# Kernel tuning notes

Hardware: AMD Instinct MI355X
Metric: run time of the kernel (lower is better)

The kernel has to match this reference:

```python
import jax, jax.numpy as jnp
import numpy as np

B, M, P, L, L_EVAL = 16, 32, 16, 1024, 2048


def setup_inputs() -> dict:
    key = jax.random.key(0)
    ks = jax.random.split(key, 6)
    # sorted event times per (B, P) path via cumsum of positive steps
    steps = jax.random.uniform(ks[0], (B, P, L), minval=0.01, maxval=0.1)
    event_times = jnp.cumsum(steps, axis=-1)  # [B, P, L], strictly increasing
    norm_constants = jax.random.uniform(ks[1], (B,), minval=0.5, maxval=1.5)
    # queries on the ORIGINAL (unnormalised) time axis, spanning the event range
    t_max = event_times[..., -1]  # [B, P]
    q_norm = jax.random.uniform(ks[2], (B, P, L_EVAL)) * (1.05 * t_max)[..., None]
    query_times = q_norm * norm_constants[:, None, None]
    mu = jax.random.uniform(ks[3], (B, M, P, L), minval=0.05, maxval=1.0)
    alpha = jax.random.uniform(ks[4], (B, M, P, L), minval=0.05, maxval=2.0)
    beta = jax.random.uniform(ks[5], (B, M, P, L), minval=0.1, maxval=3.0)
    return {
        "query_times": query_times,
        "event_times": event_times,
        "mu": mu,
        "alpha": alpha,
        "beta": beta,
        "norm_constants": norm_constants,
    }


def _batched_searchsorted(a, v):
    # a: [B, P, L] sorted along last dim, v: [B, P, Q] -> int32 [B, P, Q]
    f = lambda av, vv: jnp.searchsorted(av, vv, side="left")
    return jax.vmap(jax.vmap(f))(a, v)


def reference(query_times, event_times, mu, alpha, beta, norm_constants):
    Bq, Pq, Le = query_times.shape
    Mm = mu.shape[1]
    # normalized_times=False path: map queries onto the normalised axis
    q_norm = query_times / norm_constants[:, None, None]  # [B, P, Le]
    # index of the latest event strictly before each query time
    last_idx = _batched_searchsorted(event_times, q_norm) - 1  # [B, P, Le]
    idx = jnp.clip(last_idx, 0, None)
    gidx = jnp.broadcast_to(idx[:, None, :, :], (Bq, Mm, Pq, Le))
    mu_last = jnp.take_along_axis(mu, gidx, axis=3)
    alpha_last = jnp.take_along_axis(alpha, gidx, axis=3)
    beta_last = jnp.take_along_axis(beta, gidx, axis=3)
    t_last = jnp.take_along_axis(event_times, idx, axis=2)  # [B, P, Le]
    t_last = jnp.where(last_idx == -1, jnp.zeros_like(t_last), t_last)
    delta_t = (q_norm - t_last)[:, None, :, :]  # [B, 1, P, Le]
    intensity = mu_last + (alpha_last - mu_last) * jnp.exp(-beta_last * delta_t)
    # map intensity back to the original scale
    intensity = intensity / norm_constants[:, None, None, None]
    return intensity
```

## Files before the change

### kernel.cpp

```cpp
#include <hip/hip_runtime.h>


constexpr int B  = 16;
constexpr int M  = 32;
constexpr int P  = 16;
constexpr int L  = 1024;
constexpr int LE = 2048;

__global__ __launch_bounds__(1024)
void hawkes_kernel(const float* __restrict__ qt,
                   const float* __restrict__ ev,
                   const float* __restrict__ mu,
                   const float* __restrict__ al,
                   const float* __restrict__ be,
                   const float* __restrict__ nc,
                   float* __restrict__ out)
{
    __shared__ float  s_ev[L];
    __shared__ float4 s_prm[2][L];

    const int bp = blockIdx.x;
    const int b  = bp >> 4;
    const int p  = bp & (P - 1);
    const int t  = threadIdx.x;

    const float norm     = nc[b];
    const float inv_norm = (float)(1.0 / (double)norm);

    const size_t row0 = ((size_t)b * M * P + p) * L;
    const size_t mstr = (size_t)P * L;

    const float e_in = ev[(size_t)bp * L + t];
    float rA_mu = mu[row0 + t],        rA_al = al[row0 + t],        rA_be = be[row0 + t];
    float rB_mu = mu[row0 + mstr + t], rB_al = al[row0 + mstr + t], rB_be = be[row0 + mstr + t];

    s_ev[t]     = e_in;
    s_prm[0][t] = make_float4(rA_mu, rA_al, rA_be, 0.0f);

    __syncthreads();

    const float2 q2 = *reinterpret_cast<const float2*>(qt + (size_t)bp * LE + 2 * t);
    int   idx0, idx1;
    float dt0, dt1;
    {
        float qn[2] = { __fmul_rn(q2.x, inv_norm), __fmul_rn(q2.y, inv_norm) };
        int lo[2] = {0, 0}, hi[2] = {L, L};
#pragma unroll
        for (int s = 0; s < 11; ++s) {
#pragma unroll
            for (int k = 0; k < 2; ++k) {
                if (lo[k] < hi[k]) {
                    const int mid = (lo[k] + hi[k]) >> 1;
                    if (s_ev[mid] < qn[k]) lo[k] = mid + 1; else hi[k] = mid;
                }
            }
        }
        const int l0 = lo[0] - 1, l1 = lo[1] - 1;
        idx0 = (l0 < 0) ? 0 : l0;   dt0 = qn[0] - ((l0 < 0) ? 0.0f : s_ev[idx0]);
        idx1 = (l1 < 0) ? 0 : l1;   dt1 = qn[1] - ((l1 < 0) ? 0.0f : s_ev[idx1]);
    }

    float* const obase = out + ((size_t)b * M * P + p) * LE + 2 * t;
    const size_t ostr  = (size_t)P * LE;

#define COMPUTE_ROW(BUF, mrow)                                                  \
    {                                                                           \
        const float4 v0 = s_prm[BUF][idx0];                                     \
        const float4 v1 = s_prm[BUF][idx1];                                     \
        float2 o;                                                               \
        o.x = fmaf(v0.y - v0.x, __expf(-v0.z * dt0), v0.x) * inv_norm;          \
        o.y = fmaf(v1.y - v1.x, __expf(-v1.z * dt1), v1.x) * inv_norm;          \
        *reinterpret_cast<float2*>(obase + (size_t)(mrow) * ostr) = o;          \
    }

#pragma unroll 1
    for (int m = 0; m < M; m += 2) {
        if (m + 2 < M) {
            const size_t r = row0 + (size_t)(m + 2) * mstr;
            rA_mu = mu[r + t];  rA_al = al[r + t];  rA_be = be[r + t];
        }
        COMPUTE_ROW(0, m)
        s_prm[1][t] = make_float4(rB_mu, rB_al, rB_be, 0.0f);
        __syncthreads();

        if (m + 3 < M) {
            const size_t r = row0 + (size_t)(m + 3) * mstr;
            rB_mu = mu[r + t];  rB_al = al[r + t];  rB_be = be[r + t];
        }
        COMPUTE_ROW(1, m + 1)
        if (m + 2 < M) {
            s_prm[0][t] = make_float4(rA_mu, rA_al, rA_be, 0.0f);
        }
        __syncthreads();
    }
#undef COMPUTE_ROW
}

extern "C" void kernel_launch(void* const* d_in, const int* in_sizes, int n_in,
                              void* d_out, int out_size, void* d_ws, size_t ws_size,
                              hipStream_t stream) {
    const float* qt = (const float*)d_in[0];
    const float* ev = (const float*)d_in[1];
    const float* mu = (const float*)d_in[2];
    const float* al = (const float*)d_in[3];
    const float* be = (const float*)d_in[4];
    const float* nc = (const float*)d_in[5];
    float* out = (float*)d_out;

    hawkes_kernel<<<B * P, 1024, 0, stream>>>(qt, ev, mu, al, be, nc, out);
}
```

Baseline: 33.83 us.

## Stage four m-rows per barrier with float4 loads and SoA shared buffers

```diff
diff --git a/kernel.cpp b/kernel.cpp
--- a/kernel.cpp
+++ b/kernel.cpp
@@ -6,6 +6,10 @@
 constexpr int P  = 16;
 constexpr int L  = 1024;
 constexpr int LE = 2048;
+constexpr int RI = 4;
+constexpr int NI = M / RI;
+
+typedef float fx2 __attribute__((ext_vector_type(2)));
 
 __global__ __launch_bounds__(1024)
 void hawkes_kernel(const float* __restrict__ qt,
@@ -16,8 +20,10 @@
                    const float* __restrict__ nc,
                    float* __restrict__ out)
 {
-    __shared__ float  s_ev[L];
-    __shared__ float4 s_prm[2][L];
+    __shared__ float s_ev[L];
+    __shared__ float s_mu[2][RI][L];
+    __shared__ float s_al[2][RI][L];
+    __shared__ float s_be[2][RI][L];
 
     const int bp = blockIdx.x;
     const int b  = bp >> 4;
@@ -30,12 +36,26 @@
     const size_t row0 = ((size_t)b * M * P + p) * L;
     const size_t mstr = (size_t)P * L;
 
+    const int sr = t >> 8;
+    const int sc = (t & 255) * 4;
+    const size_t soff = (size_t)sr * mstr + sc;
+
     const float e_in = ev[(size_t)bp * L + t];
-    float rA_mu = mu[row0 + t],        rA_al = al[row0 + t],        rA_be = be[row0 + t];
-    float rB_mu = mu[row0 + mstr + t], rB_al = al[row0 + mstr + t], rB_be = be[row0 + mstr + t];
+    float4 Am, Aa, Ab, Bm, Ba, Bb;
+    Am = *reinterpret_cast<const float4*>(mu + row0 + soff);
+    Aa = *reinterpret_cast<const float4*>(al + row0 + soff);
+    Ab = *reinterpret_cast<const float4*>(be + row0 + soff);
+    {
+        const size_t r1 = row0 + (size_t)RI * mstr + soff;
+        Bm = *reinterpret_cast<const float4*>(mu + r1);
+        Ba = *reinterpret_cast<const float4*>(al + r1);
+        Bb = *reinterpret_cast<const float4*>(be + r1);
+    }
 
-    s_ev[t]     = e_in;
-    s_prm[0][t] = make_float4(rA_mu, rA_al, rA_be, 0.0f);
+    s_ev[t] = e_in;
+    *reinterpret_cast<float4*>(&s_mu[0][sr][sc]) = Am;
+    *reinterpret_cast<float4*>(&s_al[0][sr][sc]) = Aa;
+    *reinterpret_cast<float4*>(&s_be[0][sr][sc]) = Ab;
 
     __syncthreads();
 
@@ -63,37 +83,55 @@
     float* const obase = out + ((size_t)b * M * P + p) * LE + 2 * t;
     const size_t ostr  = (size_t)P * LE;
 
-#define COMPUTE_ROW(BUF, mrow)                                                  \
-    {                                                                           \
-        const float4 v0 = s_prm[BUF][idx0];                                     \
-        const float4 v1 = s_prm[BUF][idx1];                                     \
-        float2 o;                                                               \
-        o.x = fmaf(v0.y - v0.x, __expf(-v0.z * dt0), v0.x) * inv_norm;          \
-        o.y = fmaf(v1.y - v1.x, __expf(-v1.z * dt1), v1.x) * inv_norm;          \
-        *reinterpret_cast<float2*>(obase + (size_t)(mrow) * ostr) = o;          \
+#define COMPUTE_INTERVAL(BUF, mbase)                                           \
+    _Pragma("unroll")                                                          \
+    for (int mm = 0; mm < RI; ++mm) {                                          \
+        fx2 o;                                                                 \
+        {                                                                      \
+            const float m0 = s_mu[BUF][mm][idx0];                              \
+            const float a0 = s_al[BUF][mm][idx0];                              \
+            const float b0 = s_be[BUF][mm][idx0];                              \
+            o.x = fmaf(a0 - m0, __expf(-b0 * dt0), m0) * inv_norm;             \
+        }                                                                      \
+        {                                                                      \
+            const float m1 = s_mu[BUF][mm][idx1];                              \
+            const float a1 = s_al[BUF][mm][idx1];                              \
+            const float b1 = s_be[BUF][mm][idx1];                              \
+            o.y = fmaf(a1 - m1, __expf(-b1 * dt1), m1) * inv_norm;             \
+        }                                                                      \
+        __builtin_nontemporal_store(                                           \
+            o, reinterpret_cast<fx2*>(obase + (size_t)((mbase) + mm) * ostr)); \
     }
 
 #pragma unroll 1
-    for (int m = 0; m < M; m += 2) {
-        if (m + 2 < M) {
-            const size_t r = row0 + (size_t)(m + 2) * mstr;
-            rA_mu = mu[r + t];  rA_al = al[r + t];  rA_be = be[r + t];
+    for (int j = 0; j < NI / 2; ++j) {
+        if (2 * j + 2 < NI) {
+            const size_t r = row0 + (size_t)(2 * j + 2) * RI * mstr + soff;
+            Am = *reinterpret_cast<const float4*>(mu + r);
+            Aa = *reinterpret_cast<const float4*>(al + r);
+            Ab = *reinterpret_cast<const float4*>(be + r);
         }
-        COMPUTE_ROW(0, m)
-        s_prm[1][t] = make_float4(rB_mu, rB_al, rB_be, 0.0f);
+        COMPUTE_INTERVAL(0, 2 * j * RI)
+        *reinterpret_cast<float4*>(&s_mu[1][sr][sc]) = Bm;
+        *reinterpret_cast<float4*>(&s_al[1][sr][sc]) = Ba;
+        *reinterpret_cast<float4*>(&s_be[1][sr][sc]) = Bb;
         __syncthreads();
 
-        if (m + 3 < M) {
-            const size_t r = row0 + (size_t)(m + 3) * mstr;
-            rB_mu = mu[r + t];  rB_al = al[r + t];  rB_be = be[r + t];
+        if (2 * j + 3 < NI) {
+            const size_t r = row0 + (size_t)(2 * j + 3) * RI * mstr + soff;
+            Bm = *reinterpret_cast<const float4*>(mu + r);
+            Ba = *reinterpret_cast<const float4*>(al + r);
+            Bb = *reinterpret_cast<const float4*>(be + r);
         }
-        COMPUTE_ROW(1, m + 1)
-        if (m + 2 < M) {
-            s_prm[0][t] = make_float4(rA_mu, rA_al, rA_be, 0.0f);
+        COMPUTE_INTERVAL(1, (2 * j + 1) * RI)
+        if (2 * j + 2 < NI) {
+            *reinterpret_cast<float4*>(&s_mu[0][sr][sc]) = Am;
+            *reinterpret_cast<float4*>(&s_al[0][sr][sc]) = Aa;
+            *reinterpret_cast<float4*>(&s_be[0][sr][sc]) = Ab;
         }
         __syncthreads();
     }
-#undef COMPUTE_ROW
+#undef COMPUTE_INTERVAL
 }
 
 extern "C" void kernel_launch(void* const* d_in, const int* in_sizes, int n_in,
```

Result: slower. 35.69 us (+5.5%).
